# Performance work log

Hardware: AMD Instinct MI355X
Metric: run time of the kernel (lower is better)

The kernel has to match this reference:

```python
import jax, jax.numpy as jnp
import numpy as np

B, T, HID = 2, 2048, 2048
H, DQ, DV, R = 16, 128, 128, 32
DCQ, DCKV, DCO = 768, 512, 512
EPS = 1e-6
SCALE = DQ ** -0.5


def _rms(x, w):
    xf = x.astype(jnp.float32)
    var = jnp.mean(xf * xf, axis=-1, keepdims=True)
    return w * (xf * jax.lax.rsqrt(var + EPS)).astype(x.dtype)


def _rotate_half(x):
    d = x.shape[-1] // 2
    return jnp.concatenate([-x[..., d:], x[..., :d]], axis=-1)


def setup_inputs() -> dict:
    key = jax.random.key(0)
    ks = jax.random.split(key, 9)
    s = 0.02
    hidden_states = jax.random.normal(ks[0], (B, T, HID), dtype=jnp.float32)
    # RoPE tables: inv_freq over R/2 dims, duplicated (cat(freqs, freqs))
    inv_freq = 1.0 / (10000.0 ** (np.arange(0, R, 2, dtype=np.float32) / R))
    freqs = np.arange(T, dtype=np.float32)[:, None] * inv_freq[None, :]  # [T, R/2]
    emb = np.concatenate([freqs, freqs], axis=-1)  # [T, R]
    cos = jnp.asarray(np.cos(emb))
    sin = jnp.asarray(np.sin(emb))
    return {
        "hidden_states": hidden_states,
        "cos": cos,
        "sin": sin,
        "Wq_shared": jax.random.normal(ks[1], (DCQ, HID), jnp.float32) * s,
        "q_shared_norm_w": jnp.ones((DCQ,), jnp.float32),
        "Wkv_shared": jax.random.normal(ks[2], (DCKV, HID), jnp.float32) * s,
        "kv_shared_norm_w": jnp.ones((DCKV,), jnp.float32),
        "Wq_private": jax.random.normal(ks[3], (H * DQ, DCQ), jnp.float32) * s,
        "Wkv_private": jax.random.normal(ks[4], (H * (DQ + DV), DCKV), jnp.float32) * s,
        "Wg_private": jax.random.normal(ks[5], (H * DV, HID), jnp.float32) * s,
        "Wo_private": jax.random.normal(ks[6], (DCO, H * DV), jnp.float32) * s,
        "o_private_norm_w": jnp.ones((DCO,), jnp.float32),
        "Wo_shared": jax.random.normal(ks[7], (HID, DCO), jnp.float32) * s,
    }


def reference(hidden_states, cos, sin, Wq_shared, q_shared_norm_w, Wkv_shared,
              kv_shared_norm_w, Wq_private, Wkv_private, Wg_private,
              Wo_private, o_private_norm_w, Wo_shared):
    x = hidden_states
    b, t, _ = x.shape
    # shared (latent) projections + RMSNorm
    q_shared = _rms(x @ Wq_shared.T, q_shared_norm_w)    # [B,T,DCQ]
    kv_shared = _rms(x @ Wkv_shared.T, kv_shared_norm_w)  # [B,T,DCKV]
    # private per-head projections
    q = (q_shared @ Wq_private.T).reshape(b, t, H, DQ).transpose(0, 2, 1, 3)
    kv = kv_shared @ Wkv_private.T                        # [B,T,H*(DQ+DV)]
    k_flat, v_flat = jnp.split(kv, 2, axis=-1)            # keys block then values block
    gates = jax.nn.silu(x @ Wg_private.T)                 # [B,T,H*DV]
    v_flat = v_flat * gates
    k = k_flat.reshape(b, t, H, DQ).transpose(0, 2, 1, 3)
    v = v_flat.reshape(b, t, H, DV).transpose(0, 2, 1, 3)
    # partial RoPE on first R dims of each head
    c = cos[None, None]  # [1,1,T,R]
    s = sin[None, None]
    q_rope, q_pass = q[..., :R], q[..., R:]
    k_rope, k_pass = k[..., :R], k[..., R:]
    q = jnp.concatenate([q_rope * c + _rotate_half(q_rope) * s, q_pass], axis=-1)
    k = jnp.concatenate([k_rope * c + _rotate_half(k_rope) * s, k_pass], axis=-1)
    # causal attention
    scores = jnp.einsum('bhqd,bhkd->bhqk', q, k) * SCALE
    causal = jnp.tril(jnp.ones((t, t), dtype=bool))
    scores = jnp.where(causal, scores, jnp.finfo(scores.dtype).min)
    attn = jax.nn.softmax(scores, axis=-1)
    out = jnp.einsum('bhqk,bhkd->bhqd', attn, v)
    out = out.transpose(0, 2, 1, 3).reshape(b, t, H * DV)
    # output subspace: private proj -> norm -> shared proj
    out = _rms(out @ Wo_private.T, o_private_norm_w)
    return out @ Wo_shared.T
```

## Files before the change

### kernel.cpp

```cpp
#include <hip/hip_runtime.h>
#include <stdint.h>

typedef __attribute__((ext_vector_type(8))) short short8;
typedef __attribute__((ext_vector_type(4))) short sh4;
typedef __attribute__((ext_vector_type(4))) float f32x4;

__device__ __forceinline__ float bf2f(unsigned short u) {
  union { unsigned int i; float f; } v; v.i = ((unsigned int)u) << 16; return v.f;
}
__device__ __forceinline__ unsigned short f2bf(float f) {
  union { float f; unsigned int i; } v; v.f = f;
  unsigned int u = v.i;
  return (unsigned short)((u + 0x7fffu + ((u >> 16) & 1u)) >> 16);
}

#define B_SZ 2
#define T_SEQ 2048
#define NH 16
#define DH 128
#define ROPE_R 32
#define SCALE_Q 0.08838834764831845f

template <bool F>
__device__ __forceinline__ short8 ld8(const void* base, size_t idx) {
  if constexpr (F) {
    const float* p = (const float*)base + idx;
    f32x4 a = *(const f32x4*)p;
    f32x4 b = *(const f32x4*)(p + 4);
    short8 r;
    r[0] = (short)f2bf(a[0]); r[1] = (short)f2bf(a[1]);
    r[2] = (short)f2bf(a[2]); r[3] = (short)f2bf(a[3]);
    r[4] = (short)f2bf(b[0]); r[5] = (short)f2bf(b[1]);
    r[6] = (short)f2bf(b[2]); r[7] = (short)f2bf(b[3]);
    return r;
  } else {
    return *(const short8*)((const unsigned short*)base + idx);
  }
}

template <bool AF, bool BF, bool C32>
__global__ __launch_bounds__(256) void gemm_bt(
    const void* __restrict__ Ap, const void* __restrict__ Bp,
    void* __restrict__ Cp, int M, int N, int K) {
  __shared__ unsigned short Al[128][40];
  __shared__ unsigned short Bl[128][40];
  const int tid = threadIdx.x;
  const int lane = tid & 63, w = tid >> 6;
  const int wm = w >> 1, wn = w & 1;
  const int quad = lane >> 4, l16 = lane & 15;
  const int m0 = blockIdx.y * 128, n0 = blockIdx.x * 128;
  f32x4 acc[4][4];
#pragma unroll
  for (int i = 0; i < 4; ++i)
#pragma unroll
    for (int j = 0; j < 4; ++j)
#pragma unroll
      for (int r = 0; r < 4; ++r) acc[i][j][r] = 0.f;

  for (int k0 = 0; k0 < K; k0 += 32) {
    __syncthreads();
#pragma unroll
    for (int p = 0; p < 2; ++p) {
      int v = tid + p * 256;
      int row = v >> 2, kc = (v & 3) * 8;
      *(short8*)&Al[row][kc] = ld8<AF>(Ap, (size_t)(m0 + row) * K + k0 + kc);
      *(short8*)&Bl[row][kc] = ld8<BF>(Bp, (size_t)(n0 + row) * K + k0 + kc);
    }
    __syncthreads();
    short8 a[4];
#pragma unroll
    for (int i = 0; i < 4; ++i)
      a[i] = *(const short8*)&Al[wm * 64 + i * 16 + l16][quad * 8];
#pragma unroll
    for (int j = 0; j < 4; ++j) {
      short8 b = *(const short8*)&Bl[wn * 64 + j * 16 + l16][quad * 8];
#pragma unroll
      for (int i = 0; i < 4; ++i)
        acc[i][j] = __builtin_amdgcn_mfma_f32_16x16x32_bf16(a[i], b, acc[i][j], 0, 0, 0);
    }
  }
#pragma unroll
  for (int i = 0; i < 4; ++i)
#pragma unroll
    for (int j = 0; j < 4; ++j) {
      int row = m0 + wm * 64 + i * 16 + quad * 4;
      int col = n0 + wn * 64 + j * 16 + l16;
#pragma unroll
      for (int r = 0; r < 4; ++r) {
        if constexpr (C32)
          ((float*)Cp)[(size_t)(row + r) * N + col] = acc[i][j][r];
        else
          ((unsigned short*)Cp)[(size_t)(row + r) * N + col] = f2bf(acc[i][j][r]);
      }
    }
}

__device__ __forceinline__ void gload_lds16(const unsigned short* g, unsigned short* l) {
  __builtin_amdgcn_global_load_lds(
      (const __attribute__((address_space(1))) void*)g,
      (__attribute__((address_space(3))) void*)l, 16, 0, 0);
}

template <int BN, bool C32>
__global__ __launch_bounds__(256) void gemm_lds(
    const unsigned short* __restrict__ A, const unsigned short* __restrict__ Bw,
    void* __restrict__ Cp, int M, int N, int K) {
  __shared__ unsigned short Al[128][32];
  __shared__ unsigned short Bl[BN][32];
  const int tid = threadIdx.x;
  const int lane = tid & 63, w = tid >> 6;
  const int wm = w >> 1, wn = w & 1;
  const int quad = lane >> 4, l16 = lane & 15;
  const int m0 = blockIdx.y * 128, n0 = blockIdx.x * BN;
  constexpr int NJ = BN / 32;
  f32x4 acc[4][NJ];
#pragma unroll
  for (int i = 0; i < 4; ++i)
#pragma unroll
    for (int j = 0; j < NJ; ++j)
#pragma unroll
      for (int r = 0; r < 4; ++r) acc[i][j][r] = 0.f;

  for (int k0 = 0; k0 < K; k0 += 32) {
    __syncthreads();
#pragma unroll
    for (int p = 0; p < 2; ++p) {
      int c = w * 128 + p * 64 + lane;
      gload_lds16(A + (size_t)(m0 + (c >> 2)) * K + k0 + (c & 3) * 8,
                  &Al[0][0] + (size_t)(w * 128 + p * 64) * 8);
    }
#pragma unroll
    for (int p = 0; p < BN / 64; ++p) {
      int c = w * BN + p * 64 + lane;
      gload_lds16(Bw + (size_t)(n0 + (c >> 2)) * K + k0 + (c & 3) * 8,
                  &Bl[0][0] + (size_t)(w * BN + p * 64) * 8);
    }
    __syncthreads();
    short8 a[4], b[NJ];
#pragma unroll
    for (int i = 0; i < 4; ++i)
      a[i] = *(const short8*)&Al[wm * 64 + i * 16 + l16][quad * 8];
#pragma unroll
    for (int j = 0; j < NJ; ++j)
      b[j] = *(const short8*)&Bl[wn * (BN / 2) + j * 16 + l16][quad * 8];
#pragma unroll
    for (int j = 0; j < NJ; ++j)
#pragma unroll
      for (int i = 0; i < 4; ++i)
        acc[i][j] = __builtin_amdgcn_mfma_f32_16x16x32_bf16(a[i], b[j], acc[i][j], 0, 0, 0);
  }
#pragma unroll
  for (int i = 0; i < 4; ++i)
#pragma unroll
    for (int j = 0; j < NJ; ++j) {
      int row = m0 + wm * 64 + i * 16 + quad * 4;
      int col = n0 + wn * (BN / 2) + j * 16 + l16;
#pragma unroll
      for (int r = 0; r < 4; ++r) {
        if constexpr (C32)
          ((float*)Cp)[(size_t)(row + r) * N + col] = acc[i][j][r];
        else
          ((unsigned short*)Cp)[(size_t)(row + r) * N + col] = f2bf(acc[i][j][r]);
      }
    }
}

struct CvtArgs {
  const float* src[8];
  unsigned short* dst[8];
  long long n4[8];
};

__global__ __launch_bounds__(256) void cvt_multi(CvtArgs a, long long total4) {
  for (long long g = (long long)blockIdx.x * 256 + threadIdx.x; g < total4;
       g += (long long)gridDim.x * 256) {
    long long r = g;
    int s = 0;
    while (r >= a.n4[s]) { r -= a.n4[s]; ++s; }
    f32x4 v = ((const f32x4*)a.src[s])[r];
    sh4 o;
    o[0] = (short)f2bf(v[0]); o[1] = (short)f2bf(v[1]);
    o[2] = (short)f2bf(v[2]); o[3] = (short)f2bf(v[3]);
    ((sh4*)a.dst[s])[r] = o;
  }
}

__global__ __launch_bounds__(256) void rms_norm_ip(
    unsigned short* __restrict__ x, const float* __restrict__ w, int N) {
  unsigned short* row = x + (size_t)blockIdx.x * N;
  float vals[8];
  int cnt = 0;
  float ss = 0.f;
  for (int j = threadIdx.x; j < N; j += 256) {
    float v = bf2f(row[j]);
    vals[cnt++] = v;
    ss += v * v;
  }
#pragma unroll
  for (int d = 1; d < 64; d <<= 1) ss += __shfl_xor(ss, d);
  __shared__ float ws4[4];
  if ((threadIdx.x & 63) == 0) ws4[threadIdx.x >> 6] = ss;
  __syncthreads();
  float tot = ws4[0] + ws4[1] + ws4[2] + ws4[3];
  float scale = rsqrtf(tot / (float)N + 1e-6f);
  cnt = 0;
  for (int j = threadIdx.x; j < N; j += 256)
    row[j] = f2bf(w[j] * vals[cnt++] * scale);
}

__global__ __launch_bounds__(256) void prep_qk(
    const unsigned short* __restrict__ q_all, const unsigned short* __restrict__ k_all,
    const float* __restrict__ cosb, const float* __restrict__ sinb,
    unsigned short* __restrict__ Q, unsigned short* __restrict__ K) {
  const int bt = blockIdx.x;
  const int b = bt >> 11, t = bt & (T_SEQ - 1);
  const unsigned short* qr = q_all + (size_t)bt * (NH * DH);
  const unsigned short* kr = k_all + (size_t)bt * (NH * DH);
  for (int d = threadIdx.x; d < NH * DH; d += 256) {
    int h = d >> 7, dd = d & 127;
    float qv = bf2f(qr[d]);
    float kv = bf2f(kr[d]);
    if (dd < ROPE_R) {
      float c = cosb[t * ROPE_R + dd];
      float s = sinb[t * ROPE_R + dd];
      float qrot = (dd < 16) ? -bf2f(qr[d + 16]) : bf2f(qr[d - 16]);
      float krot = (dd < 16) ? -bf2f(kr[d + 16]) : bf2f(kr[d - 16]);
      qv = qv * c + qrot * s;
      kv = kv * c + krot * s;
    }
    size_t o = ((size_t)(b * NH + h) * T_SEQ + t) * DH + dd;
    Q[o] = f2bf(qv * SCALE_Q);
    K[o] = f2bf(kv);
  }
}

__global__ __launch_bounds__(256) void prep_vt(
    const unsigned short* __restrict__ v_all, const unsigned short* __restrict__ gates,
    unsigned short* __restrict__ Vt) {
  __shared__ unsigned short tile[64][130];
  const int bh = blockIdx.y, b = bh >> 4, h = bh & 15;
  const int t0 = blockIdx.x * 64;
  for (int idx = threadIdx.x; idx < 64 * 128; idx += 256) {
    int tt = idx >> 7, dd = idx & 127;
    size_t rowbase = (size_t)(b * T_SEQ + t0 + tt);
    float v = bf2f(v_all[rowbase * (NH * DH) + h * DH + dd]);
    float g = bf2f(gates[rowbase * (NH * DH) + h * DH + dd]);
    float sg = g / (1.f + __expf(-g));
    tile[tt][dd] = f2bf(v * sg);
  }
  __syncthreads();
  for (int idx = threadIdx.x; idx < 64 * 128; idx += 256) {
    int dd = idx >> 6, tt = idx & 63;
    Vt[((size_t)bh * DH + dd) * T_SEQ + t0 + tt] = tile[tt][dd];
  }
}

__device__ __forceinline__ void attn_update(
    const unsigned short (*Kl)[132], const unsigned short (*Vl)[68],
    unsigned short (*Pw)[96], const short8* qf, int qt, int kb, bool diag,
    int wt, int quad, int l16, f32x4* O, float* m_run, float* l_run) {
  f32x4 sc[4];
  __builtin_amdgcn_s_setprio(1);
#pragma unroll
  for (int jt = 0; jt < 4; ++jt) {
#pragma unroll
    for (int r = 0; r < 4; ++r) sc[jt][r] = 0.f;
#pragma unroll
    for (int kk = 0; kk < 4; ++kk) {
      short8 kf = *(const short8*)&Kl[jt * 16 + l16][kk * 32 + quad * 8];
      sc[jt] = __builtin_amdgcn_mfma_f32_16x16x32_bf16(qf[kk], kf, sc[jt], 0, 0, 0);
    }
  }
  __builtin_amdgcn_s_setprio(0);
  if (diag) {
#pragma unroll
    for (int jt = 0; jt < 4; ++jt) {
      int key = kb + jt * 16 + l16;
#pragma unroll
      for (int r = 0; r < 4; ++r) {
        int row = qt * 64 + wt * 16 + quad * 4 + r;
        if (key > row) sc[jt][r] = -1e30f;
      }
    }
  }
  float alpha[4], psum[4];
#pragma unroll
  for (int r = 0; r < 4; ++r) {
    float mx = fmaxf(fmaxf(sc[0][r], sc[1][r]), fmaxf(sc[2][r], sc[3][r]));
    mx = fmaxf(mx, __shfl_xor(mx, 1)); mx = fmaxf(mx, __shfl_xor(mx, 2));
    mx = fmaxf(mx, __shfl_xor(mx, 4)); mx = fmaxf(mx, __shfl_xor(mx, 8));
    float mnew = fmaxf(m_run[r], mx);
    alpha[r] = __expf(m_run[r] - mnew);
    m_run[r] = mnew;
    psum[r] = 0.f;
  }
#pragma unroll
  for (int jt = 0; jt < 4; ++jt)
#pragma unroll
    for (int r = 0; r < 4; ++r) {
      float p = __expf(sc[jt][r] - m_run[r]);
      sc[jt][r] = p;
      psum[r] += p;
    }
#pragma unroll
  for (int r = 0; r < 4; ++r) {
    float s = psum[r];
    s += __shfl_xor(s, 1); s += __shfl_xor(s, 2);
    s += __shfl_xor(s, 4); s += __shfl_xor(s, 8);
    l_run[r] = l_run[r] * alpha[r] + s;
  }
#pragma unroll
  for (int jn = 0; jn < 8; ++jn)
#pragma unroll
    for (int r = 0; r < 4; ++r) O[jn][r] *= alpha[r];
#pragma unroll
  for (int jt = 0; jt < 4; ++jt)
#pragma unroll
    for (int r = 0; r < 4; ++r)
      Pw[quad * 4 + r][jt * 16 + l16] = f2bf(sc[jt][r]);
  short8 pa[2];
#pragma unroll
  for (int kk = 0; kk < 2; ++kk)
    pa[kk] = *(const short8*)&Pw[l16][kk * 32 + quad * 8];
  __builtin_amdgcn_s_setprio(1);
#pragma unroll
  for (int jn = 0; jn < 8; ++jn) {
#pragma unroll
    for (int kk = 0; kk < 2; ++kk) {
      short8 vf = *(const short8*)&Vl[jn * 16 + l16][kk * 32 + quad * 8];
      O[jn] = __builtin_amdgcn_mfma_f32_16x16x32_bf16(pa[kk], vf, O[jn], 0, 0, 0);
    }
  }
  __builtin_amdgcn_s_setprio(0);
}

__global__ __launch_bounds__(512, 4) void flash_attn(
    const unsigned short* __restrict__ Q, const unsigned short* __restrict__ K,
    const unsigned short* __restrict__ Vt, unsigned short* __restrict__ Out) {
  __shared__ unsigned short Kl[64][132];
  __shared__ unsigned short Vl[128][68];
  __shared__ unsigned short P_lds[8][16][96];
  const int l = blockIdx.x;
  const int s = l & 7, qq = l >> 3;
  const int bh = s + 8 * (qq >> 4);
  const int qp = qq & 15;
  const int qa = qp, qb = 31 - qp;
  const int b = bh >> 4, h = bh & 15;
  const int tid = threadIdx.x;
  const int lane = tid & 63, w = tid >> 6;
  const int wt = w & 3;
  const bool isB = w >= 4;
  const int myq = isB ? qb : qa;
  const int quad = lane >> 4, l16 = lane & 15;
  const unsigned short* Qb = Q + (size_t)bh * T_SEQ * DH;
  const unsigned short* Kb = K + (size_t)bh * T_SEQ * DH;
  const unsigned short* Vb = Vt + (size_t)bh * DH * T_SEQ;

  short8 qf[4];
  const int qrow = myq * 64 + wt * 16 + l16;
#pragma unroll
  for (int kk = 0; kk < 4; ++kk)
    qf[kk] = *(const short8*)&Qb[(size_t)qrow * DH + kk * 32 + quad * 8];

  f32x4 O[8];
  float m_run[4], l_run[4];
#pragma unroll
  for (int jn = 0; jn < 8; ++jn)
#pragma unroll
    for (int r = 0; r < 4; ++r) O[jn][r] = 0.f;
#pragma unroll
  for (int r = 0; r < 4; ++r) { m_run[r] = -1e30f; l_run[r] = 0.f; }

  short8 krg[2], vrg[2];
#pragma unroll
  for (int p = 0; p < 2; ++p) {
    int id = tid + p * 512;
    krg[p] = *(const short8*)&Kb[(size_t)(id >> 4) * DH + (id & 15) * 8];
    vrg[p] = *(const short8*)&Vb[(size_t)(id >> 3) * T_SEQ + (id & 7) * 8];
  }
#pragma unroll
  for (int p = 0; p < 2; ++p) {
    int id = tid + p * 512;
    *(short8*)&Kl[id >> 4][(id & 15) * 8] = krg[p];
    *(short8*)&Vl[id >> 3][(id & 7) * 8] = vrg[p];
  }
  __syncthreads();

  const int last = qb;
  for (int kt = 0; kt <= last; ++kt) {
    const int kb = kt * 64;
    if (kt < last) {
      const int nb = kb + 64;
#pragma unroll
      for (int p = 0; p < 2; ++p) {
        int id = tid + p * 512;
        krg[p] = *(const short8*)&Kb[(size_t)(nb + (id >> 4)) * DH + (id & 15) * 8];
        vrg[p] = *(const short8*)&Vb[(size_t)(id >> 3) * T_SEQ + nb + (id & 7) * 8];
      }
    }
    if (isB || kt <= qa)
      attn_update(Kl, Vl, P_lds[w], qf, myq, kb, kt == (isB ? last : qa),
                  wt, quad, l16, O, m_run, l_run);
    if (kt < last) {
      __syncthreads();
#pragma unroll
      for (int p = 0; p < 2; ++p) {
        int id = tid + p * 512;
        *(short8*)&Kl[id >> 4][(id & 15) * 8] = krg[p];
        *(short8*)&Vl[id >> 3][(id & 7) * 8] = vrg[p];
      }
      __syncthreads();
    }
  }

#pragma unroll
  for (int jn = 0; jn < 8; ++jn)
#pragma unroll
    for (int r = 0; r < 4; ++r) {
      int rr = myq * 64 + wt * 16 + quad * 4 + r;
      Out[((size_t)(b * T_SEQ) + rr) * (NH * DH) + h * DH + jn * 16 + l16] =
          f2bf(O[jn][r] / l_run[r]);
    }
}

extern "C" void kernel_launch(void* const* d_in, const int* in_sizes, int n_in,
                              void* d_out, int out_size, void* d_ws, size_t ws_size,
                              hipStream_t stream) {
  const void*  x     = d_in[0];
  const float* cosb  = (const float*)d_in[1];
  const float* sinb  = (const float*)d_in[2];
  const void*  Wq_s  = d_in[3];
  const float* qs_w  = (const float*)d_in[4];
  const void*  Wkv_s = d_in[5];
  const float* kvs_w = (const float*)d_in[6];
  const void*  Wq_p  = d_in[7];
  const float* Wkv_p = (const float*)d_in[8];
  const void*  Wg_p  = d_in[9];
  const void*  Wo_p  = d_in[10];
  const float* o_w   = (const float*)d_in[11];
  const void*  Wo_s  = d_in[12];
  (void)in_sizes; (void)n_in; (void)out_size;

  const int M = B_SZ * T_SEQ;
  char* ws = (char*)d_ws;
  unsigned short* qs    = (unsigned short*)(ws + 0);
  unsigned short* omid  = qs;
  unsigned short* kvs   = (unsigned short*)(ws + 6291456);
  unsigned short* gates = (unsigned short*)(ws + 10485760);
  unsigned short* k_all = gates;
  unsigned short* v_all = (unsigned short*)(ws + 27262976);
  unsigned short* Qb    = v_all;
  unsigned short* Vt    = (unsigned short*)(ws + 44040192);
  unsigned short* Kb    = (unsigned short*)(ws + 60817408);
  unsigned short* q_all = (unsigned short*)d_out;
  unsigned short* attn  = (unsigned short*)d_out;

  dim3 blk(256);
  dim3 blk512(512);
  const size_t FAST_WS_NEEDED = 119537664;

  if (ws_size >= FAST_WS_NEEDED) {
    unsigned short* xb     = (unsigned short*)(ws + 77594624);
    unsigned short* Wq_s_b = (unsigned short*)(ws + 94371840);
    unsigned short* Wkv_s_b= (unsigned short*)(ws + 97517568);
    unsigned short* Wg_p_b = (unsigned short*)(ws + 99614720);
    unsigned short* Wq_p_b = (unsigned short*)(ws + 108003328);
    unsigned short* Wkv_p_b= (unsigned short*)(ws + 111149056);
    unsigned short* Wo_p_b = (unsigned short*)(ws + 115343360);
    unsigned short* Wo_s_b = (unsigned short*)(ws + 117440512);

    CvtArgs ca;
    ca.src[0] = (const float*)x;    ca.dst[0] = xb;      ca.n4[0] = 2097152;
    ca.src[1] = (const float*)Wq_s; ca.dst[1] = Wq_s_b;  ca.n4[1] = 393216;
    ca.src[2] = (const float*)Wkv_s;ca.dst[2] = Wkv_s_b; ca.n4[2] = 262144;
    ca.src[3] = (const float*)Wg_p; ca.dst[3] = Wg_p_b;  ca.n4[3] = 1048576;
    ca.src[4] = (const float*)Wq_p; ca.dst[4] = Wq_p_b;  ca.n4[4] = 393216;
    ca.src[5] = Wkv_p;              ca.dst[5] = Wkv_p_b; ca.n4[5] = 524288;
    ca.src[6] = (const float*)Wo_p; ca.dst[6] = Wo_p_b;  ca.n4[6] = 262144;
    ca.src[7] = (const float*)Wo_s; ca.dst[7] = Wo_s_b;  ca.n4[7] = 262144;
    long long total4 = 5242880;
    cvt_multi<<<dim3(2048), blk, 0, stream>>>(ca, total4);

    gemm_lds<128, false><<<dim3(768 / 128, M / 128), blk, 0, stream>>>(xb, Wq_s_b, qs, M, 768, 2048);
    gemm_lds<64,  false><<<dim3(512 / 64,  M / 128), blk, 0, stream>>>(xb, Wkv_s_b, kvs, M, 512, 2048);
    gemm_lds<128, false><<<dim3(2048 / 128, M / 128), blk, 0, stream>>>(xb, Wg_p_b, gates, M, 2048, 2048);
    rms_norm_ip<<<M, blk, 0, stream>>>(qs, qs_w, 768);
    rms_norm_ip<<<M, blk, 0, stream>>>(kvs, kvs_w, 512);
    gemm_lds<128, false><<<dim3(2048 / 128, M / 128), blk, 0, stream>>>(qs, Wq_p_b, q_all, M, 2048, 768);
    gemm_lds<128, false><<<dim3(2048 / 128, M / 128), blk, 0, stream>>>(
        kvs, Wkv_p_b + (size_t)2048 * 512, v_all, M, 2048, 512);
    prep_vt<<<dim3(T_SEQ / 64, B_SZ * NH), blk, 0, stream>>>(v_all, gates, Vt);
    gemm_lds<128, false><<<dim3(2048 / 128, M / 128), blk, 0, stream>>>(kvs, Wkv_p_b, k_all, M, 2048, 512);
    prep_qk<<<M, blk, 0, stream>>>(q_all, k_all, cosb, sinb, Qb, Kb);
    flash_attn<<<dim3(512), blk512, 0, stream>>>(Qb, Kb, Vt, attn);
    gemm_lds<64,  false><<<dim3(512 / 64, M / 128), blk, 0, stream>>>(attn, Wo_p_b, omid, M, 512, 2048);
    rms_norm_ip<<<M, blk, 0, stream>>>(omid, o_w, 512);
    gemm_lds<128, true><<<dim3(2048 / 128, M / 128), blk, 0, stream>>>(omid, Wo_s_b, d_out, M, 2048, 512);
  } else {
    gemm_bt<true, true, false><<<dim3(768 / 128, M / 128), blk, 0, stream>>>(x, Wq_s, qs, M, 768, 2048);
    gemm_bt<true, true, false><<<dim3(512 / 128, M / 128), blk, 0, stream>>>(x, Wkv_s, kvs, M, 512, 2048);
    gemm_bt<true, true, false><<<dim3(2048 / 128, M / 128), blk, 0, stream>>>(x, Wg_p, gates, M, 2048, 2048);
    rms_norm_ip<<<M, blk, 0, stream>>>(qs, qs_w, 768);
    rms_norm_ip<<<M, blk, 0, stream>>>(kvs, kvs_w, 512);
    gemm_bt<false, true, false><<<dim3(2048 / 128, M / 128), blk, 0, stream>>>(qs, Wq_p, q_all, M, 2048, 768);
    gemm_bt<false, true, false><<<dim3(2048 / 128, M / 128), blk, 0, stream>>>(
        kvs, Wkv_p + (size_t)2048 * 512, v_all, M, 2048, 512);
    prep_vt<<<dim3(T_SEQ / 64, B_SZ * NH), blk, 0, stream>>>(v_all, gates, Vt);
    gemm_bt<false, true, false><<<dim3(2048 / 128, M / 128), blk, 0, stream>>>(kvs, Wkv_p, k_all, M, 2048, 512);
    prep_qk<<<M, blk, 0, stream>>>(q_all, k_all, cosb, sinb, Qb, Kb);
    flash_attn<<<dim3(512), blk512, 0, stream>>>(Qb, Kb, Vt, attn);
    gemm_bt<false, true, false><<<dim3(512 / 128, M / 128), blk, 0, stream>>>(attn, Wo_p, omid, M, 512, 2048);
    rms_norm_ip<<<M, blk, 0, stream>>>(omid, o_w, 512);
    gemm_bt<false, true, true><<<dim3(2048 / 128, M / 128), blk, 0, stream>>>(omid, Wo_s, d_out, M, 2048, 512);
  }
}
```

Before: 729.5 us.

## Read K/V straight from global memory in attention and add lazy softmax rescale

The flash attention kernel stops staging K and V tiles in shared memory. Each wave now loads its MFMA operands directly from global memory, which removes the block-wide barriers and lets each wave run its own causal range without waiting for the other half of the block. It also adds a conditional rescale: when the new tile maxima stay within a threshold of the running max across the whole wave, the max update, alpha exponentials and O rescaling are skipped. The cost is more global and L2 traffic, since the 8 waves each fetch K/V with no LDS reuse, plus a divergent branch in the softmax.

```diff
diff --git a/kernel.cpp b/kernel.cpp
--- a/kernel.cpp
+++ b/kernel.cpp
@@ -256,7 +256,7 @@
 }
 
 __device__ __forceinline__ void attn_update(
-    const unsigned short (*Kl)[132], const unsigned short (*Vl)[68],
+    const unsigned short* __restrict__ Kb, const unsigned short* __restrict__ Vb,
     unsigned short (*Pw)[96], const short8* qf, int qt, int kb, bool diag,
     int wt, int quad, int l16, f32x4* O, float* m_run, float* l_run) {
   f32x4 sc[4];
@@ -267,7 +267,7 @@
     for (int r = 0; r < 4; ++r) sc[jt][r] = 0.f;
 #pragma unroll
     for (int kk = 0; kk < 4; ++kk) {
-      short8 kf = *(const short8*)&Kl[jt * 16 + l16][kk * 32 + quad * 8];
+      short8 kf = *(const short8*)&Kb[(size_t)(kb + jt * 16 + l16) * DH + kk * 32 + quad * 8];
       sc[jt] = __builtin_amdgcn_mfma_f32_16x16x32_bf16(qf[kk], kf, sc[jt], 0, 0, 0);
     }
   }
@@ -283,36 +283,62 @@
       }
     }
   }
-  float alpha[4], psum[4];
-#pragma unroll
-  for (int r = 0; r < 4; ++r) {
-    float mx = fmaxf(fmaxf(sc[0][r], sc[1][r]), fmaxf(sc[2][r], sc[3][r]));
-    mx = fmaxf(mx, __shfl_xor(mx, 1)); mx = fmaxf(mx, __shfl_xor(mx, 2));
-    mx = fmaxf(mx, __shfl_xor(mx, 4)); mx = fmaxf(mx, __shfl_xor(mx, 8));
-    float mnew = fmaxf(m_run[r], mx);
-    alpha[r] = __expf(m_run[r] - mnew);
-    m_run[r] = mnew;
-    psum[r] = 0.f;
-  }
-#pragma unroll
-  for (int jt = 0; jt < 4; ++jt)
+  float pmax[4], psum[4];
+#pragma unroll
+  for (int r = 0; r < 4; ++r)
+    pmax[r] = fmaxf(fmaxf(sc[0][r], sc[1][r]), fmaxf(sc[2][r], sc[3][r]));
+  bool near = (pmax[0] <= m_run[0] + 8.f) & (pmax[1] <= m_run[1] + 8.f) &
+              (pmax[2] <= m_run[2] + 8.f) & (pmax[3] <= m_run[3] + 8.f);
+  if (__all((int)near)) {
+#pragma unroll
+    for (int r = 0; r < 4; ++r) psum[r] = 0.f;
+#pragma unroll
+    for (int jt = 0; jt < 4; ++jt)
+#pragma unroll
+      for (int r = 0; r < 4; ++r) {
+        float p = __expf(sc[jt][r] - m_run[r]);
+        sc[jt][r] = p;
+        psum[r] += p;
+      }
 #pragma unroll
     for (int r = 0; r < 4; ++r) {
-      float p = __expf(sc[jt][r] - m_run[r]);
-      sc[jt][r] = p;
-      psum[r] += p;
-    }
-#pragma unroll
-  for (int r = 0; r < 4; ++r) {
-    float s = psum[r];
-    s += __shfl_xor(s, 1); s += __shfl_xor(s, 2);
-    s += __shfl_xor(s, 4); s += __shfl_xor(s, 8);
-    l_run[r] = l_run[r] * alpha[r] + s;
-  }
-#pragma unroll
-  for (int jn = 0; jn < 8; ++jn)
-#pragma unroll
-    for (int r = 0; r < 4; ++r) O[jn][r] *= alpha[r];
+      float s = psum[r];
+      s += __shfl_xor(s, 1); s += __shfl_xor(s, 2);
+      s += __shfl_xor(s, 4); s += __shfl_xor(s, 8);
+      l_run[r] += s;
+    }
+  } else {
+    float alpha[4];
+#pragma unroll
+    for (int r = 0; r < 4; ++r) {
+      float mx = pmax[r];
+      mx = fmaxf(mx, __shfl_xor(mx, 1)); mx = fmaxf(mx, __shfl_xor(mx, 2));
+      mx = fmaxf(mx, __shfl_xor(mx, 4)); mx = fmaxf(mx, __shfl_xor(mx, 8));
+      float mnew = fmaxf(m_run[r], mx);
+      alpha[r] = __expf(m_run[r] - mnew);
+      m_run[r] = mnew;
+      psum[r] = 0.f;
+    }
+#pragma unroll
+    for (int jt = 0; jt < 4; ++jt)
+#pragma unroll
+      for (int r = 0; r < 4; ++r) {
+        float p = __expf(sc[jt][r] - m_run[r]);
+        sc[jt][r] = p;
+        psum[r] += p;
+      }
+#pragma unroll
+    for (int r = 0; r < 4; ++r) {
+      float s = psum[r];
+      s += __shfl_xor(s, 1); s += __shfl_xor(s, 2);
+      s += __shfl_xor(s, 4); s += __shfl_xor(s, 8);
+      l_run[r] = l_run[r] * alpha[r] + s;
+    }
+#pragma unroll
+    for (int jn = 0; jn < 8; ++jn)
+#pragma unroll
+      for (int r = 0; r < 4; ++r) O[jn][r] *= alpha[r];
+  }
 #pragma unroll
   for (int jt = 0; jt < 4; ++jt)
 #pragma unroll
@@ -327,7 +353,7 @@
   for (int jn = 0; jn < 8; ++jn) {
 #pragma unroll
     for (int kk = 0; kk < 2; ++kk) {
-      short8 vf = *(const short8*)&Vl[jn * 16 + l16][kk * 32 + quad * 8];
+      short8 vf = *(const short8*)&Vb[(size_t)(jn * 16 + l16) * T_SEQ + kb + kk * 32 + quad * 8];
       O[jn] = __builtin_amdgcn_mfma_f32_16x16x32_bf16(pa[kk], vf, O[jn], 0, 0, 0);
     }
   }
@@ -337,8 +363,6 @@
 __global__ __launch_bounds__(512, 4) void flash_attn(
     const unsigned short* __restrict__ Q, const unsigned short* __restrict__ K,
     const unsigned short* __restrict__ Vt, unsigned short* __restrict__ Out) {
-  __shared__ unsigned short Kl[64][132];
-  __shared__ unsigned short Vl[128][68];
   __shared__ unsigned short P_lds[8][16][96];
   const int l = blockIdx.x;
   const int s = l & 7, qq = l >> 3;
@@ -371,47 +395,10 @@
 #pragma unroll
   for (int r = 0; r < 4; ++r) { m_run[r] = -1e30f; l_run[r] = 0.f; }
 
-  short8 krg[2], vrg[2];
-#pragma unroll
-  for (int p = 0; p < 2; ++p) {
-    int id = tid + p * 512;
-    krg[p] = *(const short8*)&Kb[(size_t)(id >> 4) * DH + (id & 15) * 8];
-    vrg[p] = *(const short8*)&Vb[(size_t)(id >> 3) * T_SEQ + (id & 7) * 8];
-  }
-#pragma unroll
-  for (int p = 0; p < 2; ++p) {
-    int id = tid + p * 512;
-    *(short8*)&Kl[id >> 4][(id & 15) * 8] = krg[p];
-    *(short8*)&Vl[id >> 3][(id & 7) * 8] = vrg[p];
-  }
-  __syncthreads();
-
-  const int last = qb;
-  for (int kt = 0; kt <= last; ++kt) {
-    const int kb = kt * 64;
-    if (kt < last) {
-      const int nb = kb + 64;
-#pragma unroll
-      for (int p = 0; p < 2; ++p) {
-        int id = tid + p * 512;
-        krg[p] = *(const short8*)&Kb[(size_t)(nb + (id >> 4)) * DH + (id & 15) * 8];
-        vrg[p] = *(const short8*)&Vb[(size_t)(id >> 3) * T_SEQ + nb + (id & 7) * 8];
-      }
-    }
-    if (isB || kt <= qa)
-      attn_update(Kl, Vl, P_lds[w], qf, myq, kb, kt == (isB ? last : qa),
-                  wt, quad, l16, O, m_run, l_run);
-    if (kt < last) {
-      __syncthreads();
-#pragma unroll
-      for (int p = 0; p < 2; ++p) {
-        int id = tid + p * 512;
-        *(short8*)&Kl[id >> 4][(id & 15) * 8] = krg[p];
-        *(short8*)&Vl[id >> 3][(id & 7) * 8] = vrg[p];
-      }
-      __syncthreads();
-    }
-  }
+  const int my_last = myq;
+  for (int kt = 0; kt <= my_last; ++kt)
+    attn_update(Kb, Vb, P_lds[w], qf, myq, kt * 64, kt == my_last,
+                wt, quad, l16, O, m_run, l_run);
 
 #pragma unroll
   for (int jn = 0; jn < 8; ++jn)
```

After: 717.1 us. No clear change (-1.7%).

## Transpose attention MFMAs to keep P in registers with lazy softmax rescale

Applied to the files above, without the earlier changes.

Swaps the MFMA operand order so the score and output tiles come out transposed, with each lane owning one query row. This removes the per-row shuffle reductions and the P round-trip through LDS, which is replaced by cross-lane shuffles to build the PV operand. It also adds a conditional rescale that skips the O/l update unless the tile max grows past the running max by more than a threshold, and changes launch bounds to 2 blocks per CU. Vectorized 4-wide output stores are added. Risks include extra shuffle cost, higher register pressure, and lower occupancy.

```diff
diff --git a/kernel.cpp b/kernel.cpp
--- a/kernel.cpp
+++ b/kernel.cpp
@@ -257,8 +257,8 @@
 
 __device__ __forceinline__ void attn_update(
     const unsigned short (*Kl)[132], const unsigned short (*Vl)[68],
-    unsigned short (*Pw)[96], const short8* qf, int qt, int kb, bool diag,
-    int wt, int quad, int l16, f32x4* O, float* m_run, float* l_run) {
+    const short8* qf, int qrow, int kb, bool diag,
+    int quad, int l16, f32x4* O, float& m_run, float& l_part) {
   f32x4 sc[4];
   __builtin_amdgcn_s_setprio(1);
 #pragma unroll
@@ -268,78 +268,87 @@
 #pragma unroll
     for (int kk = 0; kk < 4; ++kk) {
       short8 kf = *(const short8*)&Kl[jt * 16 + l16][kk * 32 + quad * 8];
-      sc[jt] = __builtin_amdgcn_mfma_f32_16x16x32_bf16(qf[kk], kf, sc[jt], 0, 0, 0);
+      sc[jt] = __builtin_amdgcn_mfma_f32_16x16x32_bf16(kf, qf[kk], sc[jt], 0, 0, 0);
     }
   }
   __builtin_amdgcn_s_setprio(0);
   if (diag) {
 #pragma unroll
-    for (int jt = 0; jt < 4; ++jt) {
-      int key = kb + jt * 16 + l16;
+    for (int jt = 0; jt < 4; ++jt)
 #pragma unroll
       for (int r = 0; r < 4; ++r) {
-        int row = qt * 64 + wt * 16 + quad * 4 + r;
-        if (key > row) sc[jt][r] = -1e30f;
+        int key = kb + jt * 16 + quad * 4 + r;
+        if (key > qrow) sc[jt][r] = -1e30f;
       }
-    }
-  }
-  float alpha[4], psum[4];
-#pragma unroll
-  for (int r = 0; r < 4; ++r) {
-    float mx = fmaxf(fmaxf(sc[0][r], sc[1][r]), fmaxf(sc[2][r], sc[3][r]));
-    mx = fmaxf(mx, __shfl_xor(mx, 1)); mx = fmaxf(mx, __shfl_xor(mx, 2));
-    mx = fmaxf(mx, __shfl_xor(mx, 4)); mx = fmaxf(mx, __shfl_xor(mx, 8));
-    float mnew = fmaxf(m_run[r], mx);
-    alpha[r] = __expf(m_run[r] - mnew);
-    m_run[r] = mnew;
-    psum[r] = 0.f;
+  }
+  f32x4 t4 = sc[0];
+#pragma unroll
+  for (int jt = 1; jt < 4; ++jt)
+#pragma unroll
+    for (int r = 0; r < 4; ++r) t4[r] = fmaxf(t4[r], sc[jt][r]);
+  float pmax = fmaxf(fmaxf(t4[0], t4[1]), fmaxf(t4[2], t4[3]));
+  bool near = pmax <= m_run + 8.f;
+  if (!__all((int)near)) {
+    float mx = pmax;
+    mx = fmaxf(mx, __shfl_xor(mx, 16));
+    mx = fmaxf(mx, __shfl_xor(mx, 32));
+    float mnew = fmaxf(m_run, mx);
+    float alpha = __expf(m_run - mnew);
+    m_run = mnew;
+    l_part *= alpha;
+#pragma unroll
+    for (int jn = 0; jn < 8; ++jn)
+#pragma unroll
+      for (int r = 0; r < 4; ++r) O[jn][r] *= alpha;
   }
 #pragma unroll
   for (int jt = 0; jt < 4; ++jt)
 #pragma unroll
     for (int r = 0; r < 4; ++r) {
-      float p = __expf(sc[jt][r] - m_run[r]);
+      float p = __expf(sc[jt][r] - m_run);
       sc[jt][r] = p;
-      psum[r] += p;
-    }
-#pragma unroll
-  for (int r = 0; r < 4; ++r) {
-    float s = psum[r];
-    s += __shfl_xor(s, 1); s += __shfl_xor(s, 2);
-    s += __shfl_xor(s, 4); s += __shfl_xor(s, 8);
-    l_run[r] = l_run[r] * alpha[r] + s;
-  }
-#pragma unroll
-  for (int jn = 0; jn < 8; ++jn)
-#pragma unroll
-    for (int r = 0; r < 4; ++r) O[jn][r] *= alpha[r];
+      l_part += p;
+    }
+  unsigned int pk[4][2];
 #pragma unroll
   for (int jt = 0; jt < 4; ++jt)
 #pragma unroll
-    for (int r = 0; r < 4; ++r)
-      Pw[quad * 4 + r][jt * 16 + l16] = f2bf(sc[jt][r]);
-  short8 pa[2];
-#pragma unroll
-  for (int kk = 0; kk < 2; ++kk)
-    pa[kk] = *(const short8*)&Pw[l16][kk * 32 + quad * 8];
+    for (int i = 0; i < 2; ++i)
+      pk[jt][i] = (unsigned int)f2bf(sc[jt][2 * i]) |
+                  ((unsigned int)f2bf(sc[jt][2 * i + 1]) << 16);
+  const int srcA = ((quad & 1) * 2) * 16 + l16;
+  const int srcB = srcA + 16;
+  const bool hisel = quad >= 2;
+  union { short8 s; unsigned int u[4]; } pb[2];
+#pragma unroll
+  for (int kk = 0; kk < 2; ++kk) {
+#pragma unroll
+    for (int i = 0; i < 2; ++i) {
+      unsigned int a0 = __shfl(pk[kk * 2][i], srcA);
+      unsigned int a1 = __shfl(pk[kk * 2 + 1][i], srcA);
+      pb[kk].u[i] = hisel ? a1 : a0;
+      unsigned int b0 = __shfl(pk[kk * 2][i], srcB);
+      unsigned int b1 = __shfl(pk[kk * 2 + 1][i], srcB);
+      pb[kk].u[2 + i] = hisel ? b1 : b0;
+    }
+  }
   __builtin_amdgcn_s_setprio(1);
 #pragma unroll
   for (int jn = 0; jn < 8; ++jn) {
 #pragma unroll
     for (int kk = 0; kk < 2; ++kk) {
       short8 vf = *(const short8*)&Vl[jn * 16 + l16][kk * 32 + quad * 8];
-      O[jn] = __builtin_amdgcn_mfma_f32_16x16x32_bf16(pa[kk], vf, O[jn], 0, 0, 0);
+      O[jn] = __builtin_amdgcn_mfma_f32_16x16x32_bf16(vf, pb[kk].s, O[jn], 0, 0, 0);
     }
   }
   __builtin_amdgcn_s_setprio(0);
 }
 
-__global__ __launch_bounds__(512, 4) void flash_attn(
+__global__ __launch_bounds__(512, 2) void flash_attn(
     const unsigned short* __restrict__ Q, const unsigned short* __restrict__ K,
     const unsigned short* __restrict__ Vt, unsigned short* __restrict__ Out) {
   __shared__ unsigned short Kl[64][132];
   __shared__ unsigned short Vl[128][68];
-  __shared__ unsigned short P_lds[8][16][96];
   const int l = blockIdx.x;
   const int s = l & 7, qq = l >> 3;
   const int bh = s + 8 * (qq >> 4);
@@ -363,13 +372,11 @@
     qf[kk] = *(const short8*)&Qb[(size_t)qrow * DH + kk * 32 + quad * 8];
 
   f32x4 O[8];
-  float m_run[4], l_run[4];
+  float m_run = -1e30f, l_part = 0.f;
 #pragma unroll
   for (int jn = 0; jn < 8; ++jn)
 #pragma unroll
     for (int r = 0; r < 4; ++r) O[jn][r] = 0.f;
-#pragma unroll
-  for (int r = 0; r < 4; ++r) { m_run[r] = -1e30f; l_run[r] = 0.f; }
 
   short8 krg[2], vrg[2];
 #pragma unroll
@@ -399,8 +406,8 @@
       }
     }
     if (isB || kt <= qa)
-      attn_update(Kl, Vl, P_lds[w], qf, myq, kb, kt == (isB ? last : qa),
-                  wt, quad, l16, O, m_run, l_run);
+      attn_update(Kl, Vl, qf, qrow, kb, kt == (isB ? last : qa),
+                  quad, l16, O, m_run, l_part);
     if (kt < last) {
       __syncthreads();
 #pragma unroll
@@ -413,14 +420,17 @@
     }
   }
 
-#pragma unroll
-  for (int jn = 0; jn < 8; ++jn)
-#pragma unroll
-    for (int r = 0; r < 4; ++r) {
-      int rr = myq * 64 + wt * 16 + quad * 4 + r;
-      Out[((size_t)(b * T_SEQ) + rr) * (NH * DH) + h * DH + jn * 16 + l16] =
-          f2bf(O[jn][r] / l_run[r]);
-    }
+  float lsum = l_part;
+  lsum += __shfl_xor(lsum, 16);
+  lsum += __shfl_xor(lsum, 32);
+  const float inv = 1.f / lsum;
+#pragma unroll
+  for (int jn = 0; jn < 8; ++jn) {
+    sh4 o4;
+#pragma unroll
+    for (int r = 0; r < 4; ++r) o4[r] = (short)f2bf(O[jn][r] * inv);
+    *(sh4*)&Out[((size_t)(b * T_SEQ) + qrow) * (NH * DH) + h * DH + jn * 16 + quad * 4] = o4;
+  }
 }
 
 extern "C" void kernel_launch(void* const* d_in, const int* in_sizes, int n_in,
```

After: 728.2 us. Within noise of the previous version (-0.2%).
